# Kernel optimization log

Hardware: AMD Instinct MI355X
Metric: run time of the kernel (lower is better)

Reference implementation:

```python
import jax, jax.numpy as jnp
import numpy as np

STATE_DIM = 128
FEATURES = 768
DT_MIN, DT_MAX = 0.001, 0.1


def setup_inputs() -> dict:
    key = jax.random.key(0)
    ks = jax.random.split(key, 8)
    B, S, F, N = 8, 4096, FEATURES, STATE_DIM
    n = jnp.arange(N, dtype=jnp.float32)
    # HiPPO-diag inits (deterministic)
    log_A_real = jnp.log(n + 0.5)
    A_imag = jnp.pi * n
    # lecun_normal: std = 1/sqrt(fan_in), fan_in = axis -2
    B_re = jax.random.normal(ks[0], (N, F), jnp.float32) / jnp.sqrt(N)
    B_im = jax.random.normal(ks[1], (N, F), jnp.float32) / jnp.sqrt(N)
    C_re = jax.random.normal(ks[2], (F, N), jnp.float32) / jnp.sqrt(F)
    C_im = jax.random.normal(ks[3], (F, N), jnp.float32) / jnp.sqrt(F)
    D = jax.random.normal(ks[4], (F,), jnp.float32)
    log_dt = jax.random.uniform(ks[5], (N,), jnp.float32,
                                minval=jnp.log(DT_MIN), maxval=jnp.log(DT_MAX))
    u = jax.random.normal(ks[6], (B, S, F), jnp.float32)
    return {"u": u, "log_A_real": log_A_real, "A_imag": A_imag,
            "B_re": B_re, "B_im": B_im, "C_re": C_re, "C_im": C_im,
            "D": D, "log_dt": log_dt}


def reference(u, log_A_real, A_imag, B_re, B_im, C_re, C_im, D, log_dt):
    B, S, F = u.shape
    N = log_A_real.shape[0]
    dt = jnp.exp(log_dt)                           # [N]
    A_diag = -jnp.exp(log_A_real) + 1j * A_imag    # [N] complex
    A_bar = jnp.exp(A_diag * dt)                   # [N] discretized A
    B_complex = B_re + 1j * B_im                   # [N, F]
    B_bar = (A_bar[:, None] - 1.0) / (A_diag[:, None] + 1e-08) * B_complex
    C_complex = C_re + 1j * C_im                   # [F, N]

    u_f = u.astype(jnp.float32)
    Bu = jnp.einsum('bsf,nf->bsn', u_f, B_bar)     # [B, S, N] complex
    A_exp = jnp.broadcast_to(A_bar[None, None, :], (B, S, N))

    def binary_operator(e1, e2):
        a1, b1 = e1
        a2, b2 = e2
        return (a1 * a2, a2 * b1 + b2)

    _, x_states = jax.lax.associative_scan(binary_operator, (A_exp, Bu), axis=1)
    y = jnp.einsum('fn,bsn->bsf', C_complex, x_states).real
    y = y + D[None, None, :] * u_f
    return y.astype(u.dtype)
```

## Files before the change

kernel.cpp:

```cpp
#include <hip/hip_runtime.h>
#include <hip/hip_bf16.h>
#include <math.h>

typedef __attribute__((ext_vector_type(8))) short short8;
typedef __attribute__((ext_vector_type(4))) float f32x4;
typedef __attribute__((ext_vector_type(4))) unsigned int uint4v;

constexpr int kF = 768;
constexpr int kN = 128;
constexpr int kB = 8;
constexpr int kS = 4096;
constexpr int kM = kB * kS;
constexpr int kChunks = 128;
constexpr int kClen = 32;

constexpr size_t kOffBw      = 4096;
constexpr size_t kOffCw      = 397312;
constexpr size_t kOffFinals  = 790528;
constexpr size_t kOffCarries = 1052672;
constexpr size_t kOffXbf     = 1314816;

__device__ __forceinline__ unsigned short f2bf(float f) {
    unsigned int u = __builtin_bit_cast(unsigned int, f);
    u += 0x7fffu + ((u >> 16) & 1u);
    return (unsigned short)(u >> 16);
}

__device__ __forceinline__ void gload16(const void* g, void* l) {
    __builtin_amdgcn_global_load_lds(
        (const __attribute__((address_space(1))) void*)g,
        (__attribute__((address_space(3))) void*)l, 16, 0, 0);
}

#define LGKM0_BAR() do { \
    asm volatile("s_waitcnt lgkmcnt(0)" ::: "memory"); \
    __builtin_amdgcn_s_barrier(); \
    __builtin_amdgcn_sched_barrier(0); \
} while (0)

__global__ __launch_bounds__(128)
void pre1(const float* __restrict__ log_A_real, const float* __restrict__ A_imag,
          const float* __restrict__ log_dt, float* __restrict__ ws) {
    int n = threadIdx.x;
    float dt = expf(log_dt[n]);
    float ar = -expf(log_A_real[n]);
    float ai = A_imag[n];
    float er = expf(ar * dt);
    float Ar = er * cosf(ai * dt);
    float Ai = er * sinf(ai * dt);
    float dr = ar + 1e-8f, di = ai;
    float inv = 1.0f / (dr * dr + di * di);
    float nr = Ar - 1.0f, ni = Ai;
    float cr = (nr * dr + ni * di) * inv;
    float ci = (ni * dr - nr * di) * inv;
    float pr = 1.f, pi = 0.f;
    for (int i = 0; i < kClen; ++i) {
        float t = pr * Ar - pi * Ai;
        pi = pr * Ai + pi * Ar;
        pr = t;
    }
    ws[n] = Ar;        ws[128 + n] = Ai;
    ws[256 + n] = pr;  ws[384 + n] = pi;
    ws[512 + n] = cr;  ws[640 + n] = ci;
}

__global__ __launch_bounds__(256)
void pre2(const float* __restrict__ B_re, const float* __restrict__ B_im,
          const float* __restrict__ wsf, unsigned short* __restrict__ bw) {
    int id = blockIdx.x * 256 + threadIdx.x;
    int c = id / kF;
    int f = id - c * kF;
    int n = c & 127;
    float cr = wsf[512 + n], ci = wsf[640 + n];
    float br = B_re[n * kF + f], bi = B_im[n * kF + f];
    float v = (c < 128) ? (cr * br - ci * bi) : (cr * bi + ci * br);
    bw[id] = f2bf(v);
}

__global__ __launch_bounds__(256)
void pre3(const float* __restrict__ C_re, const float* __restrict__ C_im,
          unsigned short* __restrict__ cw) {
    int id = blockIdx.x * 256 + threadIdx.x;
    int f = id >> 8;
    int k = id & 255;
    float v = (k < 128) ? C_re[f * kN + k] : -C_im[f * kN + (k - 128)];
    cw[id] = f2bf(v);
}

__global__ __launch_bounds__(256, 2)
void gemm1(const float* __restrict__ A,
           const unsigned short* __restrict__ W,
           float* __restrict__ Cout) {
    constexpr int K = kF, KT = K / 32;
    constexpr int SLOT = 24576;
    __shared__ __align__(16) char smem[3 * SLOT];

    const int gx = gridDim.x;
    const int nwg = gx * gridDim.y;
    const int orig = blockIdx.y * gx + blockIdx.x;
    const int cpx = nwg >> 3;
    const int sw = (orig & 7) * cpx + (orig >> 3);
    const int m0 = (sw / gx) * 128;
    const int n0 = (sw % gx) * 128;

    const int t = threadIdx.x;
    const int wave = t >> 6, lane = t & 63;
    const int wr = wave >> 1, wc = wave & 1;
    const int lr = lane & 15, lg = lane >> 4;
    const int l3 = lane >> 3, l7 = lane & 7;
    const int uswz = l7 ^ l3;

    const float* aBase = A + (size_t)(m0 + wave * 32 + l3) * K + uswz * 4;
    const unsigned short* wBase =
        W + (size_t)(n0 + wave * 32 + l3 * 2 + (uswz >> 2)) * K + (uswz & 3) * 8;

    f32x4 acc[4][4] = {};

#define G1_ISSUE(kt_, slotbase_) do { \
    const float* aT_ = aBase + (size_t)(kt_) * 32; \
    const unsigned short* wT_ = wBase + (size_t)(kt_) * 32; \
    char* sA_ = (slotbase_); \
    char* sW_ = (slotbase_) + 16384; \
    _Pragma("unroll") for (int c_ = 0; c_ < 4; ++c_) \
        gload16(aT_ + c_ * 8 * K, sA_ + (wave * 4 + c_) * 1024); \
    _Pragma("unroll") for (int c_ = 0; c_ < 2; ++c_) \
        gload16(wT_ + c_ * 16 * K, sW_ + (wave * 2 + c_) * 1024); \
} while (0)

#define G1_MMA_SLOT(slotbase_) do { \
    const char* sA_ = (slotbase_); \
    const char* sW_ = (slotbase_) + 16384; \
    short8 ah_[4], bh_[4]; \
    _Pragma("unroll") for (int i_ = 0; i_ < 4; ++i_) { \
        const int row_ = wr * 64 + i_ * 16 + lr; \
        const f32x4 fL_ = *(const f32x4*)(sA_ + row_ * 128 + (((lg * 2)     ^ (lr & 7)) * 16)); \
        const f32x4 fH_ = *(const f32x4*)(sA_ + row_ * 128 + (((lg * 2 + 1) ^ (lr & 7)) * 16)); \
        short8 v_; \
        _Pragma("unroll") for (int e_ = 0; e_ < 4; ++e_) { \
            v_[e_]     = (short)f2bf(fL_[e_]); \
            v_[4 + e_] = (short)f2bf(fH_[e_]); \
        } \
        ah_[i_] = v_; \
    } \
    _Pragma("unroll") for (int j_ = 0; j_ < 4; ++j_) { \
        const int row_ = wc * 64 + j_ * 16 + lr; \
        const int d_ = row_ >> 1; \
        const int u_ = (((lr & 1) * 4 + lg) ^ (d_ & 7)) * 16; \
        bh_[j_] = *(const short8*)(sW_ + d_ * 128 + u_); \
    } \
    _Pragma("unroll") for (int i_ = 0; i_ < 4; ++i_) \
    _Pragma("unroll") for (int j_ = 0; j_ < 4; ++j_) \
        acc[i_][j_] = __builtin_amdgcn_mfma_f32_16x16x32_bf16(ah_[i_], bh_[j_], acc[i_][j_], 0, 0, 0); \
} while (0)

    G1_ISSUE(0, smem);
    G1_ISSUE(1, smem + SLOT);

    int slot = 0;
    for (int kt = 0; kt < KT; ++kt) {
        if (kt < KT - 1) { asm volatile("s_waitcnt vmcnt(6)" ::: "memory"); }
        else             { asm volatile("s_waitcnt vmcnt(0)" ::: "memory"); }
        __builtin_amdgcn_s_barrier();
        __builtin_amdgcn_sched_barrier(0);
        char* sb = smem + slot * SLOT;
        if (kt + 2 < KT) {
            char* nb = smem + (slot == 0 ? 2 * SLOT : (slot - 1) * SLOT);
            G1_ISSUE(kt + 2, nb);
        }
        G1_MMA_SLOT(sb);
        slot = (slot == 2) ? 0 : slot + 1;
    }

#pragma unroll
    for (int i = 0; i < 4; ++i)
#pragma unroll
        for (int j = 0; j < 4; ++j) {
            const int col = n0 + wc * 64 + j * 16 + lr;
#pragma unroll
            for (int q = 0; q < 4; ++q) {
                const int row = m0 + wr * 64 + i * 16 + lg * 4 + q;
                Cout[(size_t)row * 256 + col] = acc[i][j][q];
            }
        }
#undef G1_ISSUE
#undef G1_MMA_SLOT
}

__global__ __launch_bounds__(128)
void scanA(const float* __restrict__ Bu, const float* __restrict__ wsc,
           float* __restrict__ finals) {
    int n = threadIdx.x;
    int blk = blockIdx.x;
    int b = blk >> 7, c = blk & 127;
    float Ar = wsc[n], Ai = wsc[128 + n];
    float xr = 0.f, xi = 0.f;
    size_t base = ((size_t)(b * kS + c * kClen)) * 256;
#pragma unroll 8
    for (int s = 0; s < kClen; ++s) {
        float br = Bu[base + n], bi = Bu[base + 128 + n];
        float tr = Ar * xr - Ai * xi + br;
        xi = Ar * xi + Ai * xr + bi;
        xr = tr;
        base += 256;
    }
    finals[(size_t)blk * 256 + n] = xr;
    finals[(size_t)blk * 256 + 128 + n] = xi;
}

__global__ __launch_bounds__(128)
void scanB(const float* __restrict__ finals, const float* __restrict__ ws,
           float* __restrict__ carries) {
    int n = threadIdx.x;
    int b = blockIdx.x;
    float Pr = ws[256 + n], Pi = ws[384 + n];
    float xr = 0.f, xi = 0.f;
#pragma unroll 8
    for (int c = 0; c < kChunks; ++c) {
        size_t o = ((size_t)(b * kChunks + c)) * 256;
        carries[o + n] = xr;
        carries[o + 128 + n] = xi;
        float fr = finals[o + n], fi = finals[o + 128 + n];
        float tr = Pr * xr - Pi * xi + fr;
        xi = Pr * xi + Pi * xr + fi;
        xr = tr;
    }
}

__global__ __launch_bounds__(128)
void scanC(const float* __restrict__ Bu, const float* __restrict__ wsc,
           const float* __restrict__ carries, unsigned short* __restrict__ xbf) {
    int n = threadIdx.x;
    int blk = blockIdx.x;
    int b = blk >> 7, c = blk & 127;
    float Ar = wsc[n], Ai = wsc[128 + n];
    size_t co = (size_t)blk * 256;
    float xr = carries[co + n], xi = carries[co + 128 + n];
    size_t base = ((size_t)(b * kS + c * kClen)) * 256;
#pragma unroll 4
    for (int s = 0; s < kClen; ++s) {
        float br = Bu[base + n], bi = Bu[base + 128 + n];
        float tr = Ar * xr - Ai * xi + br;
        xi = Ar * xi + Ai * xr + bi;
        xr = tr;
        xbf[base + n]       = f2bf(xr);
        xbf[base + 128 + n] = f2bf(xi);
        base += 256;
    }
}

__global__ __launch_bounds__(256, 3)
void gemm2(const unsigned short* __restrict__ A,
           const unsigned short* __restrict__ W,
           float* __restrict__ Cout,
           const float* __restrict__ Dp, const float* __restrict__ Up) {
    constexpr int K = 256, KT = 8, Nc = kF;
    __shared__ __align__(16) short As0[128 * 40];
    __shared__ __align__(16) short As1[128 * 40];
    __shared__ __align__(16) short Ws0[128 * 40];
    __shared__ __align__(16) short Ws1[128 * 40];

    const int gx = gridDim.x;
    const int nwg = gx * gridDim.y;
    const int orig = blockIdx.y * gx + blockIdx.x;
    const int cpx = nwg >> 3;
    const int sw = (orig & 7) * cpx + (orig >> 3);
    const int m0 = (sw / gx) * 128;
    const int n0 = (sw % gx) * 128;

    const int t = threadIdx.x;
    const int sr = t >> 1, sh = t & 1;

    const int wave = t >> 6, lane = t & 63;
    const int wr = wave >> 1, wc = wave & 1;
    const int lr = lane & 15, lg = lane >> 4;

    f32x4 acc[4][4] = {};

    uint4v aA0, aA1, aB0, aB1;
    uint4v wA0, wA1, wB0, wB1;
    const unsigned short* aptr = A + (size_t)(m0 + sr) * K + sh * 16;
    const unsigned short* wptr = W + (size_t)(n0 + sr) * K + sh * 16;

#define G2_LOAD(SET, kt) do { \
    const unsigned short* p_ = aptr + (kt) * 32; \
    a##SET##0 = *(const uint4v*)p_; a##SET##1 = *(const uint4v*)(p_ + 8); \
    const unsigned short* q_ = wptr + (kt) * 32; \
    w##SET##0 = *(const uint4v*)q_; w##SET##1 = *(const uint4v*)(q_ + 8); \
} while (0)

#define G2_WRITE(Asb, Wsb, a0, a1, w0, w1) do { \
    const int o_ = sr * 40 + sh * 16; \
    *(short8*)(&Asb[o_])     = *(short8*)&a0; \
    *(short8*)(&Asb[o_ + 8]) = *(short8*)&a1; \
    *(short8*)(&Wsb[o_])     = *(short8*)&w0; \
    *(short8*)(&Wsb[o_ + 8]) = *(short8*)&w1; \
} while (0)

#define G2_MMA(Asb, Wsb) do { \
    short8 ah_[4], bh_[4]; \
    _Pragma("unroll") for (int i_ = 0; i_ < 4; ++i_) { \
        ah_[i_] = *(const short8*)(&Asb[(wr * 64 + i_ * 16 + lr) * 40 + lg * 8]); \
        bh_[i_] = *(const short8*)(&Wsb[(wc * 64 + i_ * 16 + lr) * 40 + lg * 8]); \
    } \
    _Pragma("unroll") for (int i_ = 0; i_ < 4; ++i_) \
    _Pragma("unroll") for (int j_ = 0; j_ < 4; ++j_) \
        acc[i_][j_] = __builtin_amdgcn_mfma_f32_16x16x32_bf16(ah_[i_], bh_[j_], acc[i_][j_], 0, 0, 0); \
} while (0)

    G2_LOAD(A, 0);
    G2_LOAD(B, 1);
    for (int kt = 0; kt < KT; kt += 2) {
        G2_WRITE(As0, Ws0, aA0, aA1, wA0, wA1);
        if (kt + 2 < KT) G2_LOAD(A, kt + 2);
        LGKM0_BAR();
        G2_MMA(As0, Ws0);
        G2_WRITE(As1, Ws1, aB0, aB1, wB0, wB1);
        if (kt + 3 < KT) G2_LOAD(B, kt + 3);
        LGKM0_BAR();
        G2_MMA(As1, Ws1);
    }

#pragma unroll
    for (int i = 0; i < 4; ++i)
#pragma unroll
        for (int j = 0; j < 4; ++j) {
            const int col = n0 + wc * 64 + j * 16 + lr;
#pragma unroll
            for (int q = 0; q < 4; ++q) {
                const int row = m0 + wr * 64 + i * 16 + lg * 4 + q;
                float v = acc[i][j][q];
                v = fmaf(Dp[col], Up[(size_t)row * Nc + col], v);
                Cout[(size_t)row * Nc + col] = v;
            }
        }
#undef G2_LOAD
#undef G2_WRITE
#undef G2_MMA
}

extern "C" void kernel_launch(void* const* d_in, const int* in_sizes, int n_in,
                              void* d_out, int out_size, void* d_ws, size_t ws_size,
                              hipStream_t stream) {
    const float* u          = (const float*)d_in[0];
    const float* log_A_real = (const float*)d_in[1];
    const float* A_imag     = (const float*)d_in[2];
    const float* B_re       = (const float*)d_in[3];
    const float* B_im       = (const float*)d_in[4];
    const float* C_re       = (const float*)d_in[5];
    const float* C_im       = (const float*)d_in[6];
    const float* D          = (const float*)d_in[7];
    const float* log_dt     = (const float*)d_in[8];

    char* wsb = (char*)d_ws;
    float* wsf            = (float*)wsb;
    unsigned short* bw    = (unsigned short*)(wsb + kOffBw);
    unsigned short* cw    = (unsigned short*)(wsb + kOffCw);
    float* finals         = (float*)(wsb + kOffFinals);
    float* carries        = (float*)(wsb + kOffCarries);
    unsigned short* xbf   = (unsigned short*)(wsb + kOffXbf);
    float* y              = (float*)d_out;
    float* Bu             = (float*)d_out;

    pre1<<<1, 128, 0, stream>>>(log_A_real, A_imag, log_dt, wsf);
    pre2<<<(256 * kF) / 256, 256, 0, stream>>>(B_re, B_im, wsf, bw);
    pre3<<<(kF * 256) / 256, 256, 0, stream>>>(C_re, C_im, cw);

    gemm1<<<dim3(2, kM / 128), 256, 0, stream>>>(u, bw, Bu);

    scanA<<<kB * kChunks, 128, 0, stream>>>(Bu, wsf, finals);
    scanB<<<kB, 128, 0, stream>>>(finals, wsf, carries);
    scanC<<<kB * kChunks, 128, 0, stream>>>(Bu, wsf, carries, xbf);

    gemm2<<<dim3(kF / 128, kM / 128), 256, 0, stream>>>(xbf, cw, y, D, u);
}
```

Baseline: 101.9 us.

## Fuse scan phases with flag-based decoupled lookback and widen gemm1 to full N

Merges the three scan kernels into one that keeps each chunk's Bu values in registers. Chunks publish their local finals through release flags, and each block waits on its predecessors' flags, then recomputes its carry by walking all earlier finals with the chunk-level power P1. This removes two launches and the second read of Bu. Separately, gemm1 now uses 512-thread blocks covering all 256 output columns, so each A tile is loaded and converted to bf16 once instead of twice. The trade-offs are spin-waiting that assumes earlier blocks get scheduled first, O(c) carry work per block, and one block per CU for gemm1.

```diff
diff --git a/kernel.cpp b/kernel.cpp
--- a/kernel.cpp
+++ b/kernel.cpp
@@ -17,8 +17,8 @@
 constexpr size_t kOffBw      = 4096;
 constexpr size_t kOffCw      = 397312;
 constexpr size_t kOffFinals  = 790528;
-constexpr size_t kOffCarries = 1052672;
-constexpr size_t kOffXbf     = 1314816;
+constexpr size_t kOffFlags   = 1839104;
+constexpr size_t kOffXbf     = 1843200;
 
 __device__ __forceinline__ unsigned short f2bf(float f) {
     unsigned int u = __builtin_bit_cast(unsigned int, f);
@@ -87,32 +87,26 @@
     cw[id] = f2bf(v);
 }
 
-__global__ __launch_bounds__(256, 2)
+__global__ __launch_bounds__(512, 1)
 void gemm1(const float* __restrict__ A,
            const unsigned short* __restrict__ W,
            float* __restrict__ Cout) {
     constexpr int K = kF, KT = K / 32;
-    constexpr int SLOT = 24576;
+    constexpr int SLOT = 32768;
     __shared__ __align__(16) char smem[3 * SLOT];
 
-    const int gx = gridDim.x;
-    const int nwg = gx * gridDim.y;
-    const int orig = blockIdx.y * gx + blockIdx.x;
-    const int cpx = nwg >> 3;
-    const int sw = (orig & 7) * cpx + (orig >> 3);
-    const int m0 = (sw / gx) * 128;
-    const int n0 = (sw % gx) * 128;
+    const int m0 = blockIdx.x * 128;
 
     const int t = threadIdx.x;
     const int wave = t >> 6, lane = t & 63;
-    const int wr = wave >> 1, wc = wave & 1;
+    const int wr = wave >> 2, wc = wave & 3;
     const int lr = lane & 15, lg = lane >> 4;
     const int l3 = lane >> 3, l7 = lane & 7;
     const int uswz = l7 ^ l3;
 
-    const float* aBase = A + (size_t)(m0 + wave * 32 + l3) * K + uswz * 4;
+    const float* aBase = A + (size_t)(m0 + wave * 16 + l3) * K + uswz * 4;
     const unsigned short* wBase =
-        W + (size_t)(n0 + wave * 32 + l3 * 2 + (uswz >> 2)) * K + (uswz & 3) * 8;
+        W + (size_t)(wave * 32 + l3 * 2 + (uswz >> 2)) * K + (uswz & 3) * 8;
 
     f32x4 acc[4][4] = {};
 
@@ -121,10 +115,10 @@
     const unsigned short* wT_ = wBase + (size_t)(kt_) * 32; \
     char* sA_ = (slotbase_); \
     char* sW_ = (slotbase_) + 16384; \
-    _Pragma("unroll") for (int c_ = 0; c_ < 4; ++c_) \
-        gload16(aT_ + c_ * 8 * K, sA_ + (wave * 4 + c_) * 1024); \
-    _Pragma("unroll") for (int c_ = 0; c_ < 2; ++c_) \
-        gload16(wT_ + c_ * 16 * K, sW_ + (wave * 2 + c_) * 1024); \
+    gload16(aT_,          sA_ + (wave * 2 + 0) * 1024); \
+    gload16(aT_ + 8 * K,  sA_ + (wave * 2 + 1) * 1024); \
+    gload16(wT_,          sW_ + (wave * 2 + 0) * 1024); \
+    gload16(wT_ + 16 * K, sW_ + (wave * 2 + 1) * 1024); \
 } while (0)
 
 #define G1_MMA_SLOT(slotbase_) do { \
@@ -158,7 +152,7 @@
 
     int slot = 0;
     for (int kt = 0; kt < KT; ++kt) {
-        if (kt < KT - 1) { asm volatile("s_waitcnt vmcnt(6)" ::: "memory"); }
+        if (kt < KT - 1) { asm volatile("s_waitcnt vmcnt(4)" ::: "memory"); }
         else             { asm volatile("s_waitcnt vmcnt(0)" ::: "memory"); }
         __builtin_amdgcn_s_barrier();
         __builtin_amdgcn_sched_barrier(0);
@@ -175,7 +169,7 @@
     for (int i = 0; i < 4; ++i)
 #pragma unroll
         for (int j = 0; j < 4; ++j) {
-            const int col = n0 + wc * 64 + j * 16 + lr;
+            const int col = wc * 64 + j * 16 + lr;
 #pragma unroll
             for (int q = 0; q < 4; ++q) {
                 const int row = m0 + wr * 64 + i * 16 + lg * 4 + q;
@@ -187,64 +181,62 @@
 }
 
 __global__ __launch_bounds__(128)
-void scanA(const float* __restrict__ Bu, const float* __restrict__ wsc,
-           float* __restrict__ finals) {
-    int n = threadIdx.x;
-    int blk = blockIdx.x;
-    int b = blk >> 7, c = blk & 127;
-    float Ar = wsc[n], Ai = wsc[128 + n];
+void scanAC(const float* __restrict__ Bu, const float* __restrict__ wsf,
+            float* __restrict__ finals, unsigned int* __restrict__ flags,
+            unsigned short* __restrict__ xbf) {
+    const int n = threadIdx.x;
+    const int blk = blockIdx.x;
+    const int b = blk >> 7, c = blk & 127;
+    const float Ar = wsf[n],       Ai = wsf[128 + n];
+    const float P1r = wsf[256 + n], P1i = wsf[384 + n];
+    const size_t base = ((size_t)(b * kS + c * kClen)) * 256;
+
+    float br_[kClen], bi_[kClen];
+#pragma unroll
+    for (int s = 0; s < kClen; ++s) {
+        br_[s] = Bu[base + (size_t)s * 256 + n];
+        bi_[s] = Bu[base + (size_t)s * 256 + 128 + n];
+    }
+
     float xr = 0.f, xi = 0.f;
-    size_t base = ((size_t)(b * kS + c * kClen)) * 256;
-#pragma unroll 8
+#pragma unroll
     for (int s = 0; s < kClen; ++s) {
-        float br = Bu[base + n], bi = Bu[base + 128 + n];
-        float tr = Ar * xr - Ai * xi + br;
-        xi = Ar * xi + Ai * xr + bi;
+        float tr = Ar * xr - Ai * xi + br_[s];
+        xi = Ar * xi + Ai * xr + bi_[s];
         xr = tr;
-        base += 256;
-    }
-    finals[(size_t)blk * 256 + n] = xr;
+    }
+    finals[(size_t)blk * 256 + n]       = xr;
     finals[(size_t)blk * 256 + 128 + n] = xi;
-}
-
-__global__ __launch_bounds__(128)
-void scanB(const float* __restrict__ finals, const float* __restrict__ ws,
-           float* __restrict__ carries) {
-    int n = threadIdx.x;
-    int b = blockIdx.x;
-    float Pr = ws[256 + n], Pi = ws[384 + n];
-    float xr = 0.f, xi = 0.f;
-#pragma unroll 8
-    for (int c = 0; c < kChunks; ++c) {
-        size_t o = ((size_t)(b * kChunks + c)) * 256;
-        carries[o + n] = xr;
-        carries[o + 128 + n] = xi;
+    __threadfence();
+    __syncthreads();
+    if (n == 0)
+        __hip_atomic_store(&flags[blk], 1u, __ATOMIC_RELEASE, __HIP_MEMORY_SCOPE_AGENT);
+
+    if (n < c) {
+        const unsigned int* fp = &flags[b * kChunks + n];
+        while (__hip_atomic_load(fp, __ATOMIC_ACQUIRE, __HIP_MEMORY_SCOPE_AGENT) == 0u)
+            __builtin_amdgcn_s_sleep(2);
+        __threadfence();
+    }
+    __syncthreads();
+
+    float yr = 0.f, yi = 0.f;
+    for (int j = 0; j < c; ++j) {
+        size_t o = (size_t)(b * kChunks + j) * 256;
         float fr = finals[o + n], fi = finals[o + 128 + n];
-        float tr = Pr * xr - Pi * xi + fr;
-        xi = Pr * xi + Pi * xr + fi;
+        float tr = P1r * yr - P1i * yi + fr;
+        yi = P1r * yi + P1i * yr + fi;
+        yr = tr;
+    }
+
+    xr = yr; xi = yi;
+#pragma unroll
+    for (int s = 0; s < kClen; ++s) {
+        float tr = Ar * xr - Ai * xi + br_[s];
+        xi = Ar * xi + Ai * xr + bi_[s];
         xr = tr;
-    }
-}
-
-__global__ __launch_bounds__(128)
-void scanC(const float* __restrict__ Bu, const float* __restrict__ wsc,
-           const float* __restrict__ carries, unsigned short* __restrict__ xbf) {
-    int n = threadIdx.x;
-    int blk = blockIdx.x;
-    int b = blk >> 7, c = blk & 127;
-    float Ar = wsc[n], Ai = wsc[128 + n];
-    size_t co = (size_t)blk * 256;
-    float xr = carries[co + n], xi = carries[co + 128 + n];
-    size_t base = ((size_t)(b * kS + c * kClen)) * 256;
-#pragma unroll 4
-    for (int s = 0; s < kClen; ++s) {
-        float br = Bu[base + n], bi = Bu[base + 128 + n];
-        float tr = Ar * xr - Ai * xi + br;
-        xi = Ar * xi + Ai * xr + bi;
-        xr = tr;
-        xbf[base + n]       = f2bf(xr);
-        xbf[base + 128 + n] = f2bf(xi);
-        base += 256;
+        xbf[base + (size_t)s * 256 + n]       = f2bf(xr);
+        xbf[base + (size_t)s * 256 + 128 + n] = f2bf(xi);
     }
 }
 
@@ -356,20 +348,20 @@
     unsigned short* bw    = (unsigned short*)(wsb + kOffBw);
     unsigned short* cw    = (unsigned short*)(wsb + kOffCw);
     float* finals         = (float*)(wsb + kOffFinals);
-    float* carries        = (float*)(wsb + kOffCarries);
+    unsigned int* flags   = (unsigned int*)(wsb + kOffFlags);
     unsigned short* xbf   = (unsigned short*)(wsb + kOffXbf);
     float* y              = (float*)d_out;
     float* Bu             = (float*)d_out;
 
+    hipMemsetAsync(flags, 0, kB * kChunks * sizeof(unsigned int), stream);
+
     pre1<<<1, 128, 0, stream>>>(log_A_real, A_imag, log_dt, wsf);
     pre2<<<(256 * kF) / 256, 256, 0, stream>>>(B_re, B_im, wsf, bw);
     pre3<<<(kF * 256) / 256, 256, 0, stream>>>(C_re, C_im, cw);
 
-    gemm1<<<dim3(2, kM / 128), 256, 0, stream>>>(u, bw, Bu);
-
-    scanA<<<kB * kChunks, 128, 0, stream>>>(Bu, wsf, finals);
-    scanB<<<kB, 128, 0, stream>>>(finals, wsf, carries);
-    scanC<<<kB * kChunks, 128, 0, stream>>>(Bu, wsf, carries, xbf);
+    gemm1<<<kM / 128, 512, 0, stream>>>(u, bw, Bu);
+
+    scanAC<<<kB * kChunks, 128, 0, stream>>>(Bu, wsf, finals, flags, xbf);
 
     gemm2<<<dim3(kF / 128, kM / 128), 256, 0, stream>>>(xbf, cw, y, D, u);
 }
```

Measured after the change: 219.7 us. +115.6%, slower.

## Restructure gemm1 to 64x256 tiles with register-streamed weights, LDS only for A

Applied to the files above, without the earlier changes.

gemm1 now gives each workgroup 64 rows and all 256 output columns, so the fp32 activation tile is read from HBM once instead of twice across two column blocks. The bf16 weight fragments are loaded straight from global memory into registers, double-buffered across k-steps, and LDS is kept only for the A tile, which shrinks shared memory and may raise occupancy. The cost is more direct global traffic for the weights, which depend on cache hits, and higher register pressure. The workspace offsets for carries and xbf are also moved.

```diff
diff --git a/kernel.cpp b/kernel.cpp
--- a/kernel.cpp
+++ b/kernel.cpp
@@ -17,8 +17,8 @@
 constexpr size_t kOffBw      = 4096;
 constexpr size_t kOffCw      = 397312;
 constexpr size_t kOffFinals  = 790528;
-constexpr size_t kOffCarries = 1052672;
-constexpr size_t kOffXbf     = 1314816;
+constexpr size_t kOffCarries = 1839104;
+constexpr size_t kOffXbf     = 2887680;
 
 __device__ __forceinline__ unsigned short f2bf(float f) {
     unsigned int u = __builtin_bit_cast(unsigned int, f);
@@ -92,47 +92,44 @@
            const unsigned short* __restrict__ W,
            float* __restrict__ Cout) {
     constexpr int K = kF, KT = K / 32;
-    constexpr int SLOT = 24576;
+    constexpr int SLOT = 8192;
     __shared__ __align__(16) char smem[3 * SLOT];
 
-    const int gx = gridDim.x;
-    const int nwg = gx * gridDim.y;
-    const int orig = blockIdx.y * gx + blockIdx.x;
-    const int cpx = nwg >> 3;
-    const int sw = (orig & 7) * cpx + (orig >> 3);
-    const int m0 = (sw / gx) * 128;
-    const int n0 = (sw % gx) * 128;
+    const int m0 = blockIdx.x * 64;
 
     const int t = threadIdx.x;
     const int wave = t >> 6, lane = t & 63;
-    const int wr = wave >> 1, wc = wave & 1;
+    const int wc = wave;
     const int lr = lane & 15, lg = lane >> 4;
     const int l3 = lane >> 3, l7 = lane & 7;
     const int uswz = l7 ^ l3;
 
-    const float* aBase = A + (size_t)(m0 + wave * 32 + l3) * K + uswz * 4;
-    const unsigned short* wBase =
-        W + (size_t)(n0 + wave * 32 + l3 * 2 + (uswz >> 2)) * K + (uswz & 3) * 8;
+    const float* aBase = A + (size_t)(m0 + wave * 16 + l3) * K + uswz * 4;
+    const unsigned short* wBase = W + (size_t)(wc * 64 + lr) * K + lg * 8;
 
     f32x4 acc[4][4] = {};
+    short8 wSetA0, wSetA1, wSetA2, wSetA3;
+    short8 wSetB0, wSetB1, wSetB2, wSetB3;
 
 #define G1_ISSUE(kt_, slotbase_) do { \
     const float* aT_ = aBase + (size_t)(kt_) * 32; \
+    gload16(aT_,         (slotbase_) + (wave * 2 + 0) * 1024); \
+    gload16(aT_ + 8 * K, (slotbase_) + (wave * 2 + 1) * 1024); \
+} while (0)
+
+#define G1_WLOAD(SET, kt_) do { \
     const unsigned short* wT_ = wBase + (size_t)(kt_) * 32; \
-    char* sA_ = (slotbase_); \
-    char* sW_ = (slotbase_) + 16384; \
-    _Pragma("unroll") for (int c_ = 0; c_ < 4; ++c_) \
-        gload16(aT_ + c_ * 8 * K, sA_ + (wave * 4 + c_) * 1024); \
-    _Pragma("unroll") for (int c_ = 0; c_ < 2; ++c_) \
-        gload16(wT_ + c_ * 16 * K, sW_ + (wave * 2 + c_) * 1024); \
-} while (0)
-
-#define G1_MMA_SLOT(slotbase_) do { \
+    wSet##SET##0 = *(const short8*)(wT_); \
+    wSet##SET##1 = *(const short8*)(wT_ + 16 * K); \
+    wSet##SET##2 = *(const short8*)(wT_ + 32 * K); \
+    wSet##SET##3 = *(const short8*)(wT_ + 48 * K); \
+} while (0)
+
+#define G1_MMA(slotbase_, SET) do { \
     const char* sA_ = (slotbase_); \
-    const char* sW_ = (slotbase_) + 16384; \
-    short8 ah_[4], bh_[4]; \
+    short8 ah_[4]; \
     _Pragma("unroll") for (int i_ = 0; i_ < 4; ++i_) { \
-        const int row_ = wr * 64 + i_ * 16 + lr; \
+        const int row_ = i_ * 16 + lr; \
         const f32x4 fL_ = *(const f32x4*)(sA_ + row_ * 128 + (((lg * 2)     ^ (lr & 7)) * 16)); \
         const f32x4 fH_ = *(const f32x4*)(sA_ + row_ * 128 + (((lg * 2 + 1) ^ (lr & 7)) * 16)); \
         short8 v_; \
@@ -142,48 +139,54 @@
         } \
         ah_[i_] = v_; \
     } \
-    _Pragma("unroll") for (int j_ = 0; j_ < 4; ++j_) { \
-        const int row_ = wc * 64 + j_ * 16 + lr; \
-        const int d_ = row_ >> 1; \
-        const int u_ = (((lr & 1) * 4 + lg) ^ (d_ & 7)) * 16; \
-        bh_[j_] = *(const short8*)(sW_ + d_ * 128 + u_); \
+    _Pragma("unroll") for (int i_ = 0; i_ < 4; ++i_) { \
+        acc[i_][0] = __builtin_amdgcn_mfma_f32_16x16x32_bf16(ah_[i_], wSet##SET##0, acc[i_][0], 0, 0, 0); \
+        acc[i_][1] = __builtin_amdgcn_mfma_f32_16x16x32_bf16(ah_[i_], wSet##SET##1, acc[i_][1], 0, 0, 0); \
+        acc[i_][2] = __builtin_amdgcn_mfma_f32_16x16x32_bf16(ah_[i_], wSet##SET##2, acc[i_][2], 0, 0, 0); \
+        acc[i_][3] = __builtin_amdgcn_mfma_f32_16x16x32_bf16(ah_[i_], wSet##SET##3, acc[i_][3], 0, 0, 0); \
     } \
-    _Pragma("unroll") for (int i_ = 0; i_ < 4; ++i_) \
-    _Pragma("unroll") for (int j_ = 0; j_ < 4; ++j_) \
-        acc[i_][j_] = __builtin_amdgcn_mfma_f32_16x16x32_bf16(ah_[i_], bh_[j_], acc[i_][j_], 0, 0, 0); \
+} while (0)
+
+#define G1_SUBSTEP(kt_, CUR, NXT) do { \
+    if ((kt_) < KT - 1) { asm volatile("s_waitcnt vmcnt(6)" ::: "memory"); } \
+    else                { asm volatile("s_waitcnt vmcnt(4)" ::: "memory"); } \
+    __builtin_amdgcn_s_barrier(); \
+    __builtin_amdgcn_sched_barrier(0); \
+    char* sb_ = smem + slot * SLOT; \
+    if ((kt_) + 2 < KT) { \
+        char* nb_ = smem + (slot == 0 ? 2 * SLOT : (slot - 1) * SLOT); \
+        G1_ISSUE((kt_) + 2, nb_); \
+    } \
+    if ((kt_) + 1 < KT) G1_WLOAD(NXT, (kt_) + 1); \
+    G1_MMA(sb_, CUR); \
+    slot = (slot == 2) ? 0 : slot + 1; \
 } while (0)
 
     G1_ISSUE(0, smem);
     G1_ISSUE(1, smem + SLOT);
+    G1_WLOAD(A, 0);
 
     int slot = 0;
-    for (int kt = 0; kt < KT; ++kt) {
-        if (kt < KT - 1) { asm volatile("s_waitcnt vmcnt(6)" ::: "memory"); }
-        else             { asm volatile("s_waitcnt vmcnt(0)" ::: "memory"); }
-        __builtin_amdgcn_s_barrier();
-        __builtin_amdgcn_sched_barrier(0);
-        char* sb = smem + slot * SLOT;
-        if (kt + 2 < KT) {
-            char* nb = smem + (slot == 0 ? 2 * SLOT : (slot - 1) * SLOT);
-            G1_ISSUE(kt + 2, nb);
-        }
-        G1_MMA_SLOT(sb);
-        slot = (slot == 2) ? 0 : slot + 1;
+    for (int kt = 0; kt < KT; kt += 2) {
+        G1_SUBSTEP(kt,     A, B);
+        G1_SUBSTEP(kt + 1, B, A);
     }
 
 #pragma unroll
     for (int i = 0; i < 4; ++i)
 #pragma unroll
         for (int j = 0; j < 4; ++j) {
-            const int col = n0 + wc * 64 + j * 16 + lr;
+            const int col = wc * 64 + j * 16 + lr;
 #pragma unroll
             for (int q = 0; q < 4; ++q) {
-                const int row = m0 + wr * 64 + i * 16 + lg * 4 + q;
+                const int row = m0 + i * 16 + lg * 4 + q;
                 Cout[(size_t)row * 256 + col] = acc[i][j][q];
             }
         }
 #undef G1_ISSUE
-#undef G1_MMA_SLOT
+#undef G1_WLOAD
+#undef G1_MMA
+#undef G1_SUBSTEP
 }
 
 __global__ __launch_bounds__(128)
@@ -365,7 +368,7 @@
     pre2<<<(256 * kF) / 256, 256, 0, stream>>>(B_re, B_im, wsf, bw);
     pre3<<<(kF * 256) / 256, 256, 0, stream>>>(C_re, C_im, cw);
 
-    gemm1<<<dim3(2, kM / 128), 256, 0, stream>>>(u, bw, Bu);
+    gemm1<<<kM / 64, 256, 0, stream>>>(u, bw, Bu);
 
     scanA<<<kB * kChunks, 128, 0, stream>>>(Bu, wsf, finals);
     scanB<<<kB, 128, 0, stream>>>(finals, wsf, carries);
```

Measured after the change: 112.1 us. 1.1x slower.
